# Optimization experiments

Hardware: AMD Instinct MI355X
Metric: run time of the kernel (lower is better)

## Reference

```python
import jax, jax.numpy as jnp
import numpy as np

V = 36      # nodes per graph (3 temporal x 12 spatial)
C = 3       # temporal embedding slots
S = 12      # spatial embedding slots
F0 = 1025   # input feature width
H1, H2 = 256, 64
B = 1024    # graphs
N = B * V
DEG = 8     # random in-block neighbors per node (symmetrized -> 16 avg degree)
BN_EPS = 1e-5


def _edges(k):
    # 8 random neighbors per node within its own 36-node block, symmetrized
    nbr = jax.random.randint(k, (N, DEG), 0, V)
    block = (jnp.arange(N) // V) * V
    dst = (nbr + block[:, None]).reshape(-1)
    src = jnp.repeat(jnp.arange(N), DEG)
    return jnp.stack([jnp.concatenate([src, dst]),
                      jnp.concatenate([dst, src])]).astype(jnp.int32)


def setup_inputs() -> dict:
    k = jax.random.split(jax.random.key(0), 40)
    lin = lambda kk, i, o: (jax.random.normal(kk, (i, o), jnp.float32) / np.sqrt(i)).astype(jnp.float32)
    d = {}
    d['xF'] = jax.random.normal(k[0], (N, F0), jnp.float32)
    d['xD'] = jax.random.normal(k[1], (N, F0), jnp.float32)
    d['edge_index_F'] = _edges(k[2])
    d['edge_index_D'] = _edges(k[3])
    d['TembF'] = jax.random.normal(k[4], (C, F0), jnp.float32)
    d['SembF'] = jax.random.normal(k[5], (S, F0), jnp.float32)
    d['TembD'] = jax.random.normal(k[6], (C, F0), jnp.float32)
    d['SembD'] = jax.random.normal(k[7], (S, F0), jnp.float32)
    # ChebConv K=2 weights (Theta_0, Theta_1), biases; BatchNorm gamma/beta
    d['W0F1'] = lin(k[8], F0, H1); d['W1F1'] = lin(k[9], F0, H1); d['bF1'] = jnp.zeros((H1,), jnp.float32)
    d['gF1'] = jnp.ones((H1,), jnp.float32); d['btF1'] = jnp.zeros((H1,), jnp.float32)
    d['W0F2'] = lin(k[10], H1, H2); d['W1F2'] = lin(k[11], H1, H2); d['bF2'] = jnp.zeros((H2,), jnp.float32)
    d['gF2'] = jnp.ones((H2,), jnp.float32); d['btF2'] = jnp.zeros((H2,), jnp.float32)
    d['W0D1'] = lin(k[12], F0, H1); d['W1D1'] = lin(k[13], F0, H1); d['bD1'] = jnp.zeros((H1,), jnp.float32)
    d['gD1'] = jnp.ones((H1,), jnp.float32); d['btD1'] = jnp.zeros((H1,), jnp.float32)
    d['W0D2'] = lin(k[14], H1, H2); d['W1D2'] = lin(k[15], H1, H2); d['bD2'] = jnp.zeros((H2,), jnp.float32)
    d['gD2'] = jnp.ones((H2,), jnp.float32); d['btD2'] = jnp.zeros((H2,), jnp.float32)
    # fusion linear [256->5]; branch heads are tied-at-init clones of its halves
    Wlin = lin(k[16], 2 * (2 * H2), 5)
    blin = jnp.zeros((5,), jnp.float32)
    d['WlinF'] = Wlin[:2 * H2, :]; d['blinF'] = blin
    d['WlinD'] = Wlin[2 * H2:, :]; d['blinD'] = blin
    d['Wlin'] = Wlin; d['blin'] = blin
    return d


def _cheb(x, ei, W0, W1, b):
    # PyG ChebConv K=2, sym norm, lambda_max=2: out = x@W0 + (L_hat x)@W1 + b,
    # L_hat = -D^{-1/2} A D^{-1/2}. Transform-then-aggregate (linear, cheaper).
    n = x.shape[0]
    src, dst = ei[0], ei[1]
    deg = jax.ops.segment_sum(jnp.ones(src.shape, jnp.float32), src, n)
    dinv = jnp.where(deg > 0, jax.lax.rsqrt(jnp.maximum(deg, 1.0)), 0.0)
    w = -(dinv[src] * dinv[dst])                       # [E]
    h1 = x @ W1                                        # [N, out]
    tx1 = jax.ops.segment_sum(w[:, None] * h1[src], dst, n)  # scatter-add
    return x @ W0 + tx1 + b


def _bn_relu(x, g, bt):
    mu = x.mean(0)
    var = x.var(0)  # biased, as torch BatchNorm1d training-mode normalization
    return jax.nn.relu((x - mu) * jax.lax.rsqrt(var + BN_EPS) * g + bt)


def _branch(x, ei, Temb, Semb, W0a, W1a, ba, ga, bta, W0b, W1b, bb, gb, btb):
    n = x.shape[0]
    bsz = n // V
    x = x.reshape(bsz, C, S, F0).transpose(0, 2, 1, 3)      # [B,12,3,1025]
    x = x + Temb[None, None, :, :] + Semb[None, :, None, :]
    x = x.transpose(0, 2, 1, 3).reshape(n, F0)
    x = _bn_relu(_cheb(x, ei, W0a, W1a, ba), ga, bta)
    x = _bn_relu(_cheb(x, ei, W0b, W1b, bb), gb, btb)        # [N,64]
    # rows 12..23 of each 36-node block, pooled per graph
    idx = (jnp.arange(bsz)[:, None] * V + S + jnp.arange(S)[None, :]).reshape(-1)
    seg = jnp.repeat(jnp.arange(bsz), S)
    xs = x[idx]
    mx = jax.ops.segment_max(xs, seg, bsz)
    mn = jax.ops.segment_sum(xs, seg, bsz) / float(S)
    return jnp.concatenate([mx, mn], axis=1)                 # [B,128]


def reference(xF, xD, edge_index_F, edge_index_D, TembF, SembF, TembD, SembD,
              W0F1, W1F1, bF1, gF1, btF1, W0F2, W1F2, bF2, gF2, btF2,
              W0D1, W1D1, bD1, gD1, btD1, W0D2, W1D2, bD2, gD2, btD2,
              WlinF, blinF, WlinD, blinD, Wlin, blin):
    featF = _branch(xF, edge_index_F, TembF, SembF, W0F1, W1F1, bF1, gF1, btF1,
                    W0F2, W1F2, bF2, gF2, btF2)
    featD = _branch(xD, edge_index_D, TembD, SembD, W0D1, W1D1, bD1, gD1, btD1,
                    W0D2, W1D2, bD2, gD2, btD2)
    outF = jax.nn.softmax(featF @ WlinF + blinF, axis=-1)
    outD = jax.nn.softmax(featD @ WlinD + blinD, axis=-1)
    fusion = jnp.concatenate([featF, featD], axis=1)
    out = jax.nn.softmax(fusion @ Wlin + blin, axis=-1)
    return (outF, outD, fusion, out)
```

## Files before the change

### kernel.cpp

```cpp
#include <hip/hip_runtime.h>
#include <math.h>

#define NN    36864
#define F0    1025
#define H1D   256
#define H2D   64
#define VV    36
#define SS    12
#define BSZ   1024
#define BN_EPS 1e-5f

#define KT1   17
#define EMB_LD 1088
#define WT1_STRIDE  ((size_t)4*17*8192)
#define WT2_STRIDE  ((size_t)4*8192)

typedef __bf16 bf16x8 __attribute__((ext_vector_type(8)));
typedef __bf16 bf16x4 __attribute__((ext_vector_type(4)));
typedef float  f32x4  __attribute__((ext_vector_type(4)));

__device__ __forceinline__ float4 ld4u(const float* p) {
    float4 v;
    __builtin_memcpy(&v, p, 16);
    return v;
}

__device__ __forceinline__ float dinv_f(float d) {
    return d > 0.f ? rsqrtf(fmaxf(d, 1.f)) : 0.f;
}

__global__ __launch_bounds__(128) void k_graph(
    const int* __restrict__ eiF, const int* __restrict__ eiD,
    int E, float* __restrict__ AdjAll, float* __restrict__ stAll) {
    __shared__ float deg_s[VV];
    __shared__ float Adj_s[VV * VV];
    int b = blockIdx.x, br = blockIdx.y, t = threadIdx.x;
    const int* e0 = br ? eiD : eiF;
    const int Eh = E / 2;
    const int base = b * VV;

    if (b == 0 && br == 0)
        for (int i = t; i < 2 * (2 * H1D + 2 * H2D); i += 128) stAll[i] = 0.f;

    if (t < VV) deg_s[t] = 8.f;
    for (int i = t; i < VV * VV; i += 128) Adj_s[i] = 0.f;
    __syncthreads();

    for (int i = t; i < 288; i += 128) {
        int d = e0[Eh + b * 288 + i];
        atomicAdd(&deg_s[d - base], 1.f);
    }
    __syncthreads();

    for (int i = t; i < 576; i += 128) {
        int idx = (i < 288) ? (b * 288 + i) : (Eh + b * 288 + (i - 288));
        int s = e0[idx], d = e0[E + idx];
        float w = -dinv_f(deg_s[s - base]) * dinv_f(deg_s[d - base]);
        atomicAdd(&Adj_s[(d - base) * VV + (s - base)], w);
    }
    __syncthreads();

    float* A = AdjAll + ((size_t)br * BSZ + b) * (VV * VV);
    for (int i = t; i < VV * VV; i += 128) A[i] = Adj_s[i];
}

__global__ __launch_bounds__(256) void k_prepEmb(
    const float* __restrict__ TembF, const float* __restrict__ SembF,
    const float* __restrict__ TembD, const float* __restrict__ SembD,
    float* __restrict__ embSAll) {
    int br = blockIdx.y;
    const float* Temb = br ? TembD : TembF;
    const float* Semb = br ? SembD : SembF;
    float* out = embSAll + (size_t)br * VV * EMB_LD;
    int id = blockIdx.x * 256 + threadIdx.x;
    if (id >= VV * (EMB_LD / 4)) return;
    int lv = id / (EMB_LD / 4);
    int k0 = (id - lv * (EMB_LD / 4)) * 4;
    const float* pt = Temb + (size_t)(lv / SS) * F0;
    const float* ps = Semb + (size_t)(lv % SS) * F0;
    float4 v;
    float* vp = (float*)&v;
#pragma unroll
    for (int j = 0; j < 4; ++j) {
        int k = k0 + j;
        vp[j] = (k < F0) ? (pt[k] + ps[k]) : 0.f;
    }
    *reinterpret_cast<float4*>(out + (size_t)lv * EMB_LD + k0) = v;
}

__global__ __launch_bounds__(256) void k_prepW(
    const float* __restrict__ WaF, const float* __restrict__ WbF,
    const float* __restrict__ WaD, const float* __restrict__ WbD,
    __bf16* __restrict__ Wt, int K, int nkt, int split, int ldw, size_t brStride) {
    int br = blockIdx.y;
    const float* Wa = br ? WaD : WaF;
    const float* Wb = br ? WbD : WbF;
    __bf16* out = Wt + (size_t)br * brStride;

    int id = blockIdx.x * 256 + threadIdx.x;
    int gpc = nkt * 8;
    int c = id / gpc, gi = id - c * gpc;
    int kt = gi >> 3, g = gi & 7;
    int k0 = kt * 64 + g * 8;
    const float* src = (c < split) ? (Wa + c) : (Wb + (c - split));
    bf16x8 ov;
#pragma unroll
    for (int j = 0; j < 8; ++j) {
        int k = k0 + j;
        float v = (k < K) ? src[(size_t)k * ldw] : 0.f;
        ov[j] = (__bf16)v;
    }
    int r = c & 127, bn = c >> 7;
    size_t dst = ((size_t)(bn * nkt + kt) << 13) + r * 64 + ((g ^ (r & 7)) << 3);
    *(bf16x8*)(out + dst) = ov;
}

__global__ __launch_bounds__(512) void k_gemm1f(
    const float* __restrict__ xF, const float* __restrict__ xD,
    const float* __restrict__ embSAll,
    const __bf16* __restrict__ Wt1All,
    __bf16* __restrict__ H0All, __bf16* __restrict__ H1All) {
    __shared__ __align__(16) __bf16 As[2 * 8192];
    __shared__ __align__(16) __bf16 Bs[2 * 16384];
    const int tid = threadIdx.x;
    const int lane = tid & 63, wid = tid >> 6;

    const int flat = blockIdx.x;
    const int w = (flat & 7) * 144 + (flat >> 3);
    const int cy = w & 1;
    const int t2 = w >> 1;
    const int bm = t2 % 288;
    const int br = t2 / 288;

    const float* x    = br ? xD : xF;
    const float* embS = embSAll + (size_t)br * VV * EMB_LD;
    const __bf16* Wt = Wt1All + (size_t)br * WT1_STRIDE;
    __bf16* H0 = H0All + (size_t)br * NN * H1D;
    __bf16* H1 = H1All + (size_t)br * NN * H1D;

    const int wr = wid >> 2, wc = wid & 3;
    const int l15 = lane & 15, lg = lane >> 4;
    const int bn0 = cy * 2;

    const int kc = (lane & 15) * 4;
    const float *px[4], *pe[4];
    int dso[4];
#pragma unroll
    for (int i = 0; i < 4; ++i) {
        int r = wid * 16 + i * 4 + (lane >> 4);
        int g = bm * 128 + r;
        int lv = g % VV;
        px[i] = x + (size_t)g * F0 + kc;
        pe[i] = embS + (size_t)lv * EMB_LD + kc;
        dso[i] = r * 64 + (((kc >> 3) ^ (r & 7)) << 3) + (kc & 4);
    }

    int offA[2][4], offB[2][4];
#pragma unroll
    for (int kk = 0; kk < 2; ++kk) {
#pragma unroll
        for (int m = 0; m < 4; ++m) {
            int rowA = wr * 64 + m * 16 + l15;
            offA[kk][m] = rowA * 64 + (((kk * 4 + lg) ^ (rowA & 7)) << 3);
        }
#pragma unroll
        for (int n = 0; n < 4; ++n) {
            int col = wc * 64 + n * 16 + l15;
            offB[kk][n] = (col >> 7) * 8192 + (col & 127) * 64
                          + (((kk * 4 + lg) ^ (col & 7)) << 3);
        }
    }

    f32x4 acc[4][4];
#pragma unroll
    for (int m = 0; m < 4; ++m)
#pragma unroll
        for (int n = 0; n < 4; ++n) acc[m][n] = (f32x4){0.f, 0.f, 0.f, 0.f};

    f32x4 xa0[4], xa1[4];

    auto issueX = [&](int kt, f32x4 (&xa)[4]) {
        int ko = kt * 64, kb = ko + kc;
#pragma unroll
        for (int i = 0; i < 4; ++i) {
            if (kb + 3 < F0) {
                float4 a = ld4u(px[i] + ko);
                xa[i] = (f32x4){a.x, a.y, a.z, a.w};
            } else {
                f32x4 v = {0.f, 0.f, 0.f, 0.f};
#pragma unroll
                for (int j = 0; j < 4; ++j)
                    if (kb + j < F0) v[j] = px[i][ko + j];
                xa[i] = v;
            }
        }
    };
    auto writeA = [&](int kt, int buf, f32x4 (&xa)[4]) {
        int ko = kt * 64;
#pragma unroll
        for (int i = 0; i < 4; ++i) {
            float4 e = *reinterpret_cast<const float4*>(pe[i] + ko);
            bf16x4 wv;
            wv[0] = (__bf16)(xa[i][0] + e.x);
            wv[1] = (__bf16)(xa[i][1] + e.y);
            wv[2] = (__bf16)(xa[i][2] + e.z);
            wv[3] = (__bf16)(xa[i][3] + e.w);
            *(bf16x4*)(As + buf * 8192 + dso[i]) = wv;
        }
    };
    auto issueB = [&](int kt, int buf) {
#pragma unroll
        for (int cc = 0; cc < 4; ++cc) {
            int q = (wid * 4 + cc) * 512;
            int h = q >> 13, qi = q & 8191;
            const __bf16* src = Wt + (((size_t)(bn0 + h) * KT1 + kt) << 13)
                                + qi + (lane << 3);
            __builtin_amdgcn_global_load_lds(
                (const __attribute__((address_space(1))) void*)src,
                (__attribute__((address_space(3))) void*)(Bs + buf * 16384 + q), 16, 0, 0);
        }
    };
    auto mfmaStep = [&](int cur) {
        const __bf16* Ab = As + cur * 8192;
        const __bf16* Bb = Bs + cur * 16384;
#pragma unroll
        for (int kk = 0; kk < 2; ++kk) {
            bf16x8 af[4], bb[4];
#pragma unroll
            for (int m = 0; m < 4; ++m) af[m] = *(const bf16x8*)(Ab + offA[kk][m]);
#pragma unroll
            for (int n = 0; n < 4; ++n) bb[n] = *(const bf16x8*)(Bb + offB[kk][n]);
#pragma unroll
            for (int m = 0; m < 4; ++m)
#pragma unroll
                for (int n = 0; n < 4; ++n)
                    acc[m][n] = __builtin_amdgcn_mfma_f32_16x16x32_bf16(
                        af[m], bb[n], acc[m][n], 0, 0, 0);
        }
    };

    issueX(0, xa0);
    issueB(0, 0);
    writeA(0, 0, xa0);
    issueX(1, xa1);

    for (int kt = 0; kt < KT1; kt += 2) {
        __syncthreads();
        if (kt + 1 < KT1) issueB(kt + 1, 1);
        if (kt + 2 < KT1) issueX(kt + 2, xa0);
        mfmaStep(0);
        if (kt + 1 < KT1) writeA(kt + 1, 1, xa1);
        if (kt + 1 >= KT1) break;
        __syncthreads();
        if (kt + 2 < KT1) issueB(kt + 2, 0);
        if (kt + 3 < KT1) issueX(kt + 3, xa1);
        mfmaStep(1);
        if (kt + 2 < KT1) writeA(kt + 2, 0, xa0);
    }

    const int cr = lg * 4;
#pragma unroll
    for (int m = 0; m < 4; ++m) {
        int grow = bm * 128 + wr * 64 + m * 16 + cr;
#pragma unroll
        for (int n = 0; n < 4; ++n) {
            int gc = cy * 256 + wc * 64 + n * 16 + l15;
#pragma unroll
            for (int j = 0; j < 4; ++j) {
                int r = grow + j;
                if (gc < 256) H0[(size_t)r * H1D + gc] = (__bf16)acc[m][n][j];
                else          H1[(size_t)r * H1D + (gc - 256)] = (__bf16)acc[m][n][j];
            }
        }
    }
}

__global__ __launch_bounds__(256, 2) void k_gemm2f(
    const __bf16* __restrict__ YAll, const float* __restrict__ stAll,
    const float* __restrict__ gF, const float* __restrict__ btF,
    const float* __restrict__ gD, const float* __restrict__ btD,
    const __bf16* __restrict__ Wt2All,
    float* __restrict__ G0All, __bf16* __restrict__ G1All) {
    __shared__ __align__(16) __bf16 As[2 * 8192];
    __shared__ __align__(16) __bf16 Bs[2 * 8192];
    __shared__ float coef_s[2 * H1D];
    const int tid = threadIdx.x;
    const int lane = tid & 63, wid = tid >> 6;
    const int bm = blockIdx.x, br = blockIdx.z;
    const __bf16* Y   = YAll + (size_t)br * NN * H1D;
    const __bf16* Wt  = Wt2All + (size_t)br * WT2_STRIDE;
    float*  G0 = G0All + (size_t)br * NN * H2D;
    __bf16* G1 = G1All + (size_t)br * NN * H2D;

    {
        const float* st = stAll + (size_t)br * 2 * H1D;
        const float* g  = br ? gD : gF;
        const float* bt = br ? btD : btF;
        int c = tid;
        float mu = st[c] / (float)NN;
        float var = st[H1D + c] / (float)NN - mu * mu;
        float sA = g[c] * rsqrtf(var + BN_EPS);
        coef_s[c] = sA;
        coef_s[H1D + c] = bt[c] - mu * sA;
    }
    __syncthreads();

    const int wr = wid >> 1, wc = wid & 1;
    const int l15 = lane & 15, lg = lane >> 4;

    const int kc = (lane & 15) * 4;
    const __bf16* pyr[8];
    int dso[8];
#pragma unroll
    for (int i = 0; i < 8; ++i) {
        int r = wid * 32 + i * 4 + (lane >> 4);
        pyr[i] = Y + (size_t)(bm * 128 + r) * H1D + kc;
        dso[i] = r * 64 + (((kc >> 3) ^ (r & 7)) << 3) + (kc & 4);
    }

    int offA[2][4], offB[2][4];
#pragma unroll
    for (int kk = 0; kk < 2; ++kk)
#pragma unroll
        for (int m = 0; m < 4; ++m) {
            int rowA = wr * 64 + m * 16 + l15;
            offA[kk][m] = rowA * 64 + (((kk * 4 + lg) ^ (rowA & 7)) << 3);
            int col = wc * 64 + m * 16 + l15;
            offB[kk][m] = col * 64 + (((kk * 4 + lg) ^ (col & 7)) << 3);
        }

    f32x4 acc[4][4];
#pragma unroll
    for (int m = 0; m < 4; ++m)
#pragma unroll
        for (int n = 0; n < 4; ++n) acc[m][n] = (f32x4){0.f, 0.f, 0.f, 0.f};

    bf16x4 ya[8];

    auto issueY = [&](int kt) {
        int k0 = kt * 64;
#pragma unroll
        for (int i = 0; i < 8; ++i)
            ya[i] = *reinterpret_cast<const bf16x4*>(pyr[i] + k0);
    };
    auto writeA = [&](int kt, int buf) {
        int k0 = kt * 64;
        float4 cA = *reinterpret_cast<const float4*>(coef_s + k0 + kc);
        float4 cB = *reinterpret_cast<const float4*>(coef_s + H1D + k0 + kc);
#pragma unroll
        for (int i = 0; i < 8; ++i) {
            bf16x4 wv;
            wv[0] = (__bf16)fmaxf(fmaf((float)ya[i][0], cA.x, cB.x), 0.f);
            wv[1] = (__bf16)fmaxf(fmaf((float)ya[i][1], cA.y, cB.y), 0.f);
            wv[2] = (__bf16)fmaxf(fmaf((float)ya[i][2], cA.z, cB.z), 0.f);
            wv[3] = (__bf16)fmaxf(fmaf((float)ya[i][3], cA.w, cB.w), 0.f);
            *(bf16x4*)(As + buf * 8192 + dso[i]) = wv;
        }
    };
    auto issueB = [&](int kt, int buf) {
#pragma unroll
        for (int cc = 0; cc < 4; ++cc) {
            int q = (wid * 4 + cc) * 512;
            const __bf16* src = Wt + ((size_t)kt << 13) + q + (lane << 3);
            __builtin_amdgcn_global_load_lds(
                (const __attribute__((address_space(1))) void*)src,
                (__attribute__((address_space(3))) void*)(Bs + buf * 8192 + q), 16, 0, 0);
        }
    };

    issueB(0, 0);
    issueY(0);
    writeA(0, 0);

    for (int kt = 0; kt < 4; ++kt) {
        const int cur = kt & 1, nxt = cur ^ 1;
        __syncthreads();
        if (kt + 1 < 4) {
            issueB(kt + 1, nxt);
            issueY(kt + 1);
        }
        const __bf16* Ab = As + cur * 8192;
        const __bf16* Bb = Bs + cur * 8192;
#pragma unroll
        for (int kk = 0; kk < 2; ++kk) {
            bf16x8 af[4], bb[4];
#pragma unroll
            for (int m = 0; m < 4; ++m) af[m] = *(const bf16x8*)(Ab + offA[kk][m]);
#pragma unroll
            for (int n = 0; n < 4; ++n) bb[n] = *(const bf16x8*)(Bb + offB[kk][n]);
#pragma unroll
            for (int m = 0; m < 4; ++m)
#pragma unroll
                for (int n = 0; n < 4; ++n)
                    acc[m][n] = __builtin_amdgcn_mfma_f32_16x16x32_bf16(
                        af[m], bb[n], acc[m][n], 0, 0, 0);
        }
        if (kt + 1 < 4) writeA(kt + 1, nxt);
    }

    const int cr = lg * 4;
#pragma unroll
    for (int m = 0; m < 4; ++m) {
        int grow = bm * 128 + wr * 64 + m * 16 + cr;
#pragma unroll
        for (int n = 0; n < 4; ++n) {
            int col = wc * 64 + n * 16 + l15;
#pragma unroll
            for (int j = 0; j < 4; ++j) {
                int r = grow + j;
                if (col < 64) G0[(size_t)r * H2D + col] = acc[m][n][j];
                else          G1[(size_t)r * H2D + (col - 64)] = (__bf16)acc[m][n][j];
            }
        }
    }
}

__global__ __launch_bounds__(256) void k_combine_stats1(
    const float* __restrict__ AdjAll, const __bf16* __restrict__ H1All,
    const float* __restrict__ bF, const float* __restrict__ bD,
    __bf16* __restrict__ YAll, float* __restrict__ stAll) {
    __shared__ float Adj_s[VV * VV];
    __shared__ float red[256 * 9];
    int b = blockIdx.x, br = blockIdx.y, t = threadIdx.x;
    const float* Adj = AdjAll + ((size_t)br * BSZ + b) * (VV * VV);
    const __bf16* h1 = H1All + ((size_t)br * NN + (size_t)b * VV) * H1D;
    __bf16* yb = YAll + ((size_t)br * NN + (size_t)b * VV) * H1D;
    float* st = stAll + (size_t)br * 2 * H1D;
    const float* bias = br ? bD : bF;

    for (int e = t; e < VV * VV; e += 256) Adj_s[e] = Adj[e];
    __syncthreads();

    int c0 = (t & 63) * 4, r0 = t >> 6;
    float4 bv = *reinterpret_cast<const float4*>(bias + c0);
    float acc[9][4];
#pragma unroll
    for (int i = 0; i < 9; ++i) {
        bf16x4 y = *reinterpret_cast<const bf16x4*>(yb + (size_t)(r0 + 4 * i) * H1D + c0);
        acc[i][0] = (float)y[0] + bv.x; acc[i][1] = (float)y[1] + bv.y;
        acc[i][2] = (float)y[2] + bv.z; acc[i][3] = (float)y[3] + bv.w;
    }
#pragma unroll 4
    for (int j = 0; j < VV; ++j) {
        bf16x4 hv = *reinterpret_cast<const bf16x4*>(h1 + (size_t)j * H1D + c0);
        float h0 = (float)hv[0], h1f = (float)hv[1], h2 = (float)hv[2], h3 = (float)hv[3];
#pragma unroll
        for (int i = 0; i < 9; ++i) {
            float a = Adj_s[(r0 + 4 * i) * VV + j];
            acc[i][0] = fmaf(a, h0, acc[i][0]);
            acc[i][1] = fmaf(a, h1f, acc[i][1]);
            acc[i][2] = fmaf(a, h2, acc[i][2]);
            acc[i][3] = fmaf(a, h3, acc[i][3]);
        }
    }
    float s[4] = {0, 0, 0, 0}, s2[4] = {0, 0, 0, 0};
#pragma unroll
    for (int i = 0; i < 9; ++i) {
        bf16x4 wv;
        wv[0] = (__bf16)acc[i][0]; wv[1] = (__bf16)acc[i][1];
        wv[2] = (__bf16)acc[i][2]; wv[3] = (__bf16)acc[i][3];
        *reinterpret_cast<bf16x4*>(yb + (size_t)(r0 + 4 * i) * H1D + c0) = wv;
#pragma unroll
        for (int k = 0; k < 4; ++k) { s[k] += acc[i][k]; s2[k] += acc[i][k] * acc[i][k]; }
    }
#pragma unroll
    for (int k = 0; k < 4; ++k) { red[t * 9 + k] = s[k]; red[t * 9 + 4 + k] = s2[k]; }
    __syncthreads();
    {
        int cg = t >> 2, k = t & 3;
        float ss = 0.f, ss2 = 0.f;
#pragma unroll
        for (int q = 0; q < 4; ++q) {
            ss  += red[(q * 64 + cg) * 9 + k];
            ss2 += red[(q * 64 + cg) * 9 + 4 + k];
        }
        atomicAdd(&st[t], ss);
        atomicAdd(&st[H1D + t], ss2);
    }
}

__global__ __launch_bounds__(256) void k_combine_stats2(
    const float* __restrict__ AdjAll, const __bf16* __restrict__ G1All,
    const float* __restrict__ bF, const float* __restrict__ bD,
    float* __restrict__ YAll, float* __restrict__ stAll) {
    __shared__ float Adj_s[VV * VV];
    __shared__ float red[256 * 9];
    int b = blockIdx.x, br = blockIdx.y, t = threadIdx.x;
    const float* Adj = AdjAll + ((size_t)br * BSZ + b) * (VV * VV);
    const __bf16* g1 = G1All + ((size_t)br * NN + (size_t)b * VV) * H2D;
    float* yb = YAll + ((size_t)br * NN + (size_t)b * VV) * H2D;
    float* st = stAll + (size_t)br * 2 * H2D;
    const float* bias = br ? bD : bF;

    for (int e = t; e < VV * VV; e += 256) Adj_s[e] = Adj[e];
    __syncthreads();

    int c0 = (t & 15) * 4, r0 = t >> 4;
    int nr = (r0 < 4) ? 3 : 2;
    float4 bv = *reinterpret_cast<const float4*>(bias + c0);
    float acc[3][4];
    for (int i = 0; i < nr; ++i) {
        float4 y = *reinterpret_cast<const float4*>(yb + (size_t)(r0 + 16 * i) * H2D + c0);
        acc[i][0] = y.x + bv.x; acc[i][1] = y.y + bv.y;
        acc[i][2] = y.z + bv.z; acc[i][3] = y.w + bv.w;
    }
#pragma unroll 4
    for (int j = 0; j < VV; ++j) {
        bf16x4 hv = *reinterpret_cast<const bf16x4*>(g1 + (size_t)j * H2D + c0);
        float h0 = (float)hv[0], h1f = (float)hv[1], h2 = (float)hv[2], h3 = (float)hv[3];
        for (int i = 0; i < nr; ++i) {
            float a = Adj_s[(r0 + 16 * i) * VV + j];
            acc[i][0] = fmaf(a, h0, acc[i][0]);
            acc[i][1] = fmaf(a, h1f, acc[i][1]);
            acc[i][2] = fmaf(a, h2, acc[i][2]);
            acc[i][3] = fmaf(a, h3, acc[i][3]);
        }
    }
    float s[4] = {0, 0, 0, 0}, s2[4] = {0, 0, 0, 0};
    for (int i = 0; i < nr; ++i) {
        *reinterpret_cast<float4*>(yb + (size_t)(r0 + 16 * i) * H2D + c0) =
            make_float4(acc[i][0], acc[i][1], acc[i][2], acc[i][3]);
#pragma unroll
        for (int k = 0; k < 4; ++k) { s[k] += acc[i][k]; s2[k] += acc[i][k] * acc[i][k]; }
    }
#pragma unroll
    for (int k = 0; k < 4; ++k) { red[t * 9 + k] = s[k]; red[t * 9 + 4 + k] = s2[k]; }
    __syncthreads();
    if (t < 2 * H2D) {
        int cg = (t & 63) >> 2, k = t & 3, which = t >> 6;
        float ss = 0.f;
#pragma unroll
        for (int q = 0; q < 16; ++q) ss += red[(q * 16 + cg) * 9 + which * 4 + k];
        atomicAdd(&st[(t >> 6) * H2D + (t & 63)], ss);
    }
}

__global__ __launch_bounds__(128) void k_poolheads(
    const float* __restrict__ G0All, const float* __restrict__ st2All,
    const float* __restrict__ gF2, const float* __restrict__ btF2,
    const float* __restrict__ gD2, const float* __restrict__ btD2,
    const float* __restrict__ WlinF, const float* __restrict__ blinF,
    const float* __restrict__ WlinD, const float* __restrict__ blinD,
    const float* __restrict__ Wlin, const float* __restrict__ blin,
    float* __restrict__ out) {
    __shared__ float sF[128], sD[128], lg[24];
    int r = blockIdx.x, t = threadIdx.x;

    {
        int br = t >> 6, c = t & 63;
        const float* Y2 = G0All + (size_t)br * NN * H2D;
        const float* st = st2All + (size_t)br * 2 * H2D;
        const float* g  = br ? gD2 : gF2;
        const float* bt = br ? btD2 : btF2;
        float mu = st[c] / (float)NN;
        float var = st[H2D + c] / (float)NN - mu * mu;
        float sA = g[c] * rsqrtf(var + BN_EPS);
        float sB = bt[c] - mu * sA;
        float mx = -1e30f, sm = 0.f;
        const float* yb = Y2 + ((size_t)r * VV + SS) * H2D + c;
#pragma unroll
        for (int i = 0; i < SS; ++i) {
            float v = fmaxf(fmaf(yb[i * H2D], sA, sB), 0.f);
            mx = fmaxf(mx, v);
            sm += v;
        }
        float* feat = br ? sD : sF;
        feat[c] = mx;
        feat[64 + c] = sm * (1.f / 12.f);
    }
    __syncthreads();

    float* fus = out + 10240 + (size_t)r * 256;
    fus[t] = sF[t];
    fus[128 + t] = sD[t];
    if (t < 5) {
        float a = blinF[t];
        for (int k = 0; k < 128; ++k) a += sF[k] * WlinF[k * 5 + t];
        lg[t] = a;
    } else if (t >= 8 && t < 13) {
        int j = t - 8;
        float a = blinD[j];
        for (int k = 0; k < 128; ++k) a += sD[k] * WlinD[k * 5 + j];
        lg[8 + j] = a;
    } else if (t >= 16 && t < 21) {
        int j = t - 16;
        float a = blin[j];
        for (int k = 0; k < 128; ++k) a += sF[k] * Wlin[k * 5 + j];
        for (int k = 0; k < 128; ++k) a += sD[k] * Wlin[(128 + k) * 5 + j];
        lg[16 + j] = a;
    }
    __syncthreads();
    if (t < 15) {
        int grp = t / 5, j = t % 5;
        const float* l = &lg[grp * 8];
        float m = l[0];
#pragma unroll
        for (int k = 1; k < 5; ++k) m = fmaxf(m, l[k]);
        float den = 0.f;
#pragma unroll
        for (int k = 0; k < 5; ++k) den += expf(l[k] - m);
        float v = expf(l[j] - m) / den;
        float* dst = (grp == 0) ? out : (grp == 1 ? out + 5120 : out + 272384);
        dst[r * 5 + j] = v;
    }
}

extern "C" void kernel_launch(void* const* d_in, const int* in_sizes, int n_in,
                              void* d_out, int out_size, void* d_ws, size_t ws_size,
                              hipStream_t stream) {
    const float* xF    = (const float*)d_in[0];
    const float* xD    = (const float*)d_in[1];
    const int*   eiF   = (const int*)d_in[2];
    const int*   eiD   = (const int*)d_in[3];
    const float* TembF = (const float*)d_in[4];
    const float* SembF = (const float*)d_in[5];
    const float* TembD = (const float*)d_in[6];
    const float* SembD = (const float*)d_in[7];
    const float* W0F1  = (const float*)d_in[8];
    const float* W1F1  = (const float*)d_in[9];
    const float* bF1   = (const float*)d_in[10];
    const float* gF1   = (const float*)d_in[11];
    const float* btF1  = (const float*)d_in[12];
    const float* W0F2  = (const float*)d_in[13];
    const float* W1F2  = (const float*)d_in[14];
    const float* bF2   = (const float*)d_in[15];
    const float* gF2   = (const float*)d_in[16];
    const float* btF2  = (const float*)d_in[17];
    const float* W0D1  = (const float*)d_in[18];
    const float* W1D1  = (const float*)d_in[19];
    const float* bD1   = (const float*)d_in[20];
    const float* gD1   = (const float*)d_in[21];
    const float* btD1  = (const float*)d_in[22];
    const float* W0D2  = (const float*)d_in[23];
    const float* W1D2  = (const float*)d_in[24];
    const float* bD2   = (const float*)d_in[25];
    const float* gD2   = (const float*)d_in[26];
    const float* btD2  = (const float*)d_in[27];
    const float* WlinF = (const float*)d_in[28];
    const float* blinF = (const float*)d_in[29];
    const float* WlinD = (const float*)d_in[30];
    const float* blinD = (const float*)d_in[31];
    const float* Wlin  = (const float*)d_in[32];
    const float* blin  = (const float*)d_in[33];

    const int E = in_sizes[2] / 2;

    float* ws = (float*)d_ws;
    size_t o = 0;
    __bf16* H0bf = (__bf16*)(ws + o);   o += (size_t)2 * NN * H1D / 2;
    __bf16* H1bf = (__bf16*)(ws + o);   o += (size_t)2 * NN * H1D / 2;
    float*  G0   = ws + o;              o += (size_t)2 * NN * H2D;
    __bf16* G1bf = (__bf16*)(ws + o);   o += (size_t)2 * NN * H2D / 2;
    __bf16* Wt1  = (__bf16*)(ws + o);   o += (size_t)2 * WT1_STRIDE / 2;
    __bf16* Wt2  = (__bf16*)(ws + o);   o += (size_t)2 * WT2_STRIDE / 2;
    float*  embS = ws + o;              o += (size_t)2 * VV * EMB_LD;
    float*  Adj  = ws + o;              o += (size_t)2 * BSZ * VV * VV;
    float*  st1  = ws + o;              o += 2 * 2 * H1D;
    float*  st2  = ws + o;              o += 2 * 2 * H2D;

    k_graph<<<dim3(BSZ, 2), 128, 0, stream>>>(eiF, eiD, E, Adj, st1);
    k_prepEmb<<<dim3(39, 2), 256, 0, stream>>>(TembF, SembF, TembD, SembD, embS);
    k_prepW<<<dim3(272, 2), 256, 0, stream>>>(W0F1, W1F1, W0D1, W1D1, Wt1,
                                              F0, 17, 256, H1D, WT1_STRIDE);
    k_prepW<<<dim3(16, 2), 256, 0, stream>>>(W0F2, W1F2, W0D2, W1D2, Wt2,
                                             H1D, 4, 64, H2D, WT2_STRIDE);
    k_gemm1f<<<dim3(1152), 512, 0, stream>>>(xF, xD, embS, Wt1, H0bf, H1bf);
    k_combine_stats1<<<dim3(BSZ, 2), 256, 0, stream>>>(Adj, H1bf, bF1, bD1, H0bf, st1);
    k_gemm2f<<<dim3(288, 1, 2), 256, 0, stream>>>(H0bf, st1, gF1, btF1, gD1, btD1,
                                                  Wt2, G0, G1bf);
    k_combine_stats2<<<dim3(BSZ, 2), 256, 0, stream>>>(Adj, G1bf, bF2, bD2, G0, st2);
    k_poolheads<<<dim3(BSZ), 128, 0, stream>>>(G0, st2, gF2, btF2, gD2, btD2,
                                               WlinF, blinF, WlinD, blinD,
                                               Wlin, blin, (float*)d_out);
}
```

Before: 395.8 us.

## Prefetch embedding loads and use counted vmcnt waits in GEMM1 pipeline

Moves the embedding-row loads out of the LDS write step into a separate prefetch issued alongside the X loads, so they overlap MFMA work. The main loop replaces __syncthreads with an explicit partial s_waitcnt vmcnt(8) plus s_barrier, so the next tile's global loads stay in flight across the barrier. The odd-length K loop is peeled, and launch bounds now request two blocks per CU. The extra prefetch registers and the occupancy hint may cause spills, and the hand-set waitcnt is fragile if the number of outstanding loads changes.

```diff
diff --git a/kernel.cpp b/kernel.cpp
--- a/kernel.cpp
+++ b/kernel.cpp
@@ -115,7 +115,7 @@
     *(bf16x8*)(out + dst) = ov;
 }
 
-__global__ __launch_bounds__(512) void k_gemm1f(
+__global__ __launch_bounds__(512, 2) void k_gemm1f(
     const float* __restrict__ xF, const float* __restrict__ xD,
     const float* __restrict__ embSAll,
     const __bf16* __restrict__ Wt1All,
@@ -178,6 +178,7 @@
         for (int n = 0; n < 4; ++n) acc[m][n] = (f32x4){0.f, 0.f, 0.f, 0.f};
 
     f32x4 xa0[4], xa1[4];
+    float4 ea0[4], ea1[4];
 
     auto issueX = [&](int kt, f32x4 (&xa)[4]) {
         int ko = kt * 64, kb = ko + kc;
@@ -195,16 +196,20 @@
             }
         }
     };
-    auto writeA = [&](int kt, int buf, f32x4 (&xa)[4]) {
+    auto issueE = [&](int kt, float4 (&ea)[4]) {
         int ko = kt * 64;
 #pragma unroll
+        for (int i = 0; i < 4; ++i)
+            ea[i] = *reinterpret_cast<const float4*>(pe[i] + ko);
+    };
+    auto writeA = [&](int buf, f32x4 (&xa)[4], float4 (&ea)[4]) {
+#pragma unroll
         for (int i = 0; i < 4; ++i) {
-            float4 e = *reinterpret_cast<const float4*>(pe[i] + ko);
             bf16x4 wv;
-            wv[0] = (__bf16)(xa[i][0] + e.x);
-            wv[1] = (__bf16)(xa[i][1] + e.y);
-            wv[2] = (__bf16)(xa[i][2] + e.z);
-            wv[3] = (__bf16)(xa[i][3] + e.w);
+            wv[0] = (__bf16)(xa[i][0] + ea[i].x);
+            wv[1] = (__bf16)(xa[i][1] + ea[i].y);
+            wv[2] = (__bf16)(xa[i][2] + ea[i].z);
+            wv[3] = (__bf16)(xa[i][3] + ea[i].w);
             *(bf16x4*)(As + buf * 8192 + dso[i]) = wv;
         }
     };
@@ -239,24 +244,41 @@
         }
     };
 
-    issueX(0, xa0);
+    issueX(0, xa0); issueE(0, ea0);
+    writeA(0, xa0, ea0);
     issueB(0, 0);
-    writeA(0, 0, xa0);
-    issueX(1, xa1);
-
-    for (int kt = 0; kt < KT1; kt += 2) {
-        __syncthreads();
-        if (kt + 1 < KT1) issueB(kt + 1, 1);
-        if (kt + 2 < KT1) issueX(kt + 2, xa0);
+    issueX(1, xa1); issueE(1, ea1);
+
+    for (int kt = 0; kt + 3 <= 15; kt += 2) {
+        asm volatile("s_waitcnt vmcnt(8) lgkmcnt(0)" ::: "memory");
+        __builtin_amdgcn_sched_barrier(0);
+        __builtin_amdgcn_s_barrier();
+        __builtin_amdgcn_sched_barrier(0);
+        issueB(kt + 1, 1);
+        issueX(kt + 2, xa0); issueE(kt + 2, ea0);
         mfmaStep(0);
-        if (kt + 1 < KT1) writeA(kt + 1, 1, xa1);
-        if (kt + 1 >= KT1) break;
-        __syncthreads();
-        if (kt + 2 < KT1) issueB(kt + 2, 0);
-        if (kt + 3 < KT1) issueX(kt + 3, xa1);
+        writeA(1, xa1, ea1);
+        asm volatile("s_waitcnt vmcnt(8) lgkmcnt(0)" ::: "memory");
+        __builtin_amdgcn_sched_barrier(0);
+        __builtin_amdgcn_s_barrier();
+        __builtin_amdgcn_sched_barrier(0);
+        issueB(kt + 2, 0);
+        issueX(kt + 3, xa1); issueE(kt + 3, ea1);
         mfmaStep(1);
-        if (kt + 2 < KT1) writeA(kt + 2, 0, xa0);
-    }
+        writeA(0, xa0, ea0);
+    }
+
+    __syncthreads();
+    issueB(15, 1);
+    issueX(16, xa0); issueE(16, ea0);
+    mfmaStep(0);
+    writeA(1, xa1, ea1);
+    __syncthreads();
+    issueB(16, 0);
+    mfmaStep(1);
+    writeA(0, xa0, ea0);
+    __syncthreads();
+    mfmaStep(0);
 
     const int cr = lg * 4;
 #pragma unroll
```

Result: no change. 398.2 us (+0.6%).
